# Kernel tuning notes

Hardware: AMD Instinct MI355X
Metric: run time of the kernel (lower is better)

The kernel has to match this reference:

```python
import jax, jax.numpy as jnp
import numpy as np

N_NODES = 100000

def gcn_conv(x, W, b, row, col, n):
    # PyG GCNConv: linear transform, then symmetric-normalized aggregation
    h = x @ W  # [N, out]
    # add self loops
    sl = jnp.arange(n, dtype=row.dtype)
    r = jnp.concatenate([row, sl])
    c = jnp.concatenate([col, sl])
    deg = jax.ops.segment_sum(jnp.ones_like(c, dtype=h.dtype), c, num_segments=n)
    dinv = jnp.where(deg > 0, jax.lax.rsqrt(deg), 0.0)
    norm = dinv[r] * dinv[c]  # [E+N]
    out = jax.ops.segment_sum(h[r] * norm[:, None], c, num_segments=n)
    return out + b


def setup_inputs() -> dict:
    key = jax.random.key(0)
    k1, k2, k3, k4, k5, k6 = jax.random.split(key, 6)
    E = 1600000
    x = jax.random.normal(k1, (N_NODES, 256), dtype=jnp.float32)
    edge_index = jax.random.randint(k2, (2, E), 0, N_NODES, dtype=jnp.int64)
    # Glorot-style init for GCN weights
    W1 = jax.random.normal(k3, (256, 128), dtype=jnp.float32) / np.sqrt(256.0)
    b1 = jnp.zeros((128,), dtype=jnp.float32)
    W2 = jax.random.normal(k4, (128, 64), dtype=jnp.float32) / np.sqrt(128.0)
    b2 = jnp.zeros((64,), dtype=jnp.float32)
    return {"x": x, "edge_index": edge_index, "W1": W1, "b1": b1, "W2": W2, "b2": b2}


def reference(x, edge_index, W1, b1, W2, b2):
    row, col = edge_index[0], edge_index[1]
    h = gcn_conv(x, W1, b1, row, col, N_NODES)
    h = jax.nn.relu(h)
    z = gcn_conv(h, W2, b2, row, col, N_NODES)
    return z
```

## Files before the change

kernel.cpp:

```cpp
#include <hip/hip_runtime.h>

#define NN 100000
#define BW 256
#define NB ((NN + BW - 1) / BW)
#define CH 4096

typedef __attribute__((ext_vector_type(8))) short short8;
typedef __attribute__((ext_vector_type(4))) float f32x4;

__device__ __forceinline__ float bf2f(unsigned short u) {
    union { unsigned int i; float f; } v;
    v.i = ((unsigned int)u) << 16;
    return v.f;
}
__device__ __forceinline__ unsigned short f2bf(float f) {
    unsigned int u = __float_as_uint(f);
    unsigned int r = u + 0x7fffu + ((u >> 16) & 1u);
    return (unsigned short)(r >> 16);
}
__device__ __forceinline__ float ldf(const void* p, int i, int bf) {
    return bf ? bf2f(((const unsigned short*)p)[i]) : ((const float*)p)[i];
}
__device__ __forceinline__ int lde(const void* p, int i, int i64f) {
    return i64f ? (int)((const long long*)p)[i] : ((const int*)p)[i];
}
__device__ __forceinline__ short8 ld8bf(const void* p, size_t i, int bf) {
    if (bf) return *(const short8*)((const unsigned short*)p + i);
    const float* f = (const float*)p + i;
    f32x4 a = *(const f32x4*)f;
    f32x4 b = *(const f32x4*)(f + 4);
    short8 o;
    o[0] = (short)f2bf(a[0]); o[1] = (short)f2bf(a[1]);
    o[2] = (short)f2bf(a[2]); o[3] = (short)f2bf(a[3]);
    o[4] = (short)f2bf(b[0]); o[5] = (short)f2bf(b[1]);
    o[6] = (short)f2bf(b[2]); o[7] = (short)f2bf(b[3]);
    return o;
}

__global__ void detect_kernel(const unsigned int* __restrict__ xw,
                              const unsigned int* __restrict__ eiw,
                              int* __restrict__ flags) {
    __shared__ int s0, s1;
    int tid = threadIdx.x;
    if (tid == 0) { s0 = 0; s1 = 0; }
    __syncthreads();
    if (tid < 128) {
        unsigned int w = xw[tid];
        int e = (int)((w >> 7) & 0xFFu);
        if (e < 100 || e > 130) atomicAdd(&s0, 1);
    } else if (tid < 192) {
        if (eiw[2 * (tid - 128) + 1] == 0u) atomicAdd(&s1, 1);
    }
    __syncthreads();
    if (tid == 0) {
        flags[0] = (s0 < 16) ? 1 : 0;
        flags[1] = (s1 >= 48) ? 1 : 0;
    }
}

__global__ __launch_bounds__(512) void sort_tr_kernel(const void* __restrict__ ei, int E,
                                                      int* __restrict__ bcnt,
                                                      int* __restrict__ poff,
                                                      int* __restrict__ ebin,
                                                      const int* __restrict__ flags,
                                                      const void* __restrict__ w1,
                                                      const void* __restrict__ w2,
                                                      unsigned short* __restrict__ w1t,
                                                      unsigned short* __restrict__ w2t,
                                                      int PB) {
    __shared__ int lc[NB + 1];
    __shared__ int ls[512];
    __shared__ int sbuf[CH];
    int bid = blockIdx.x, tid = threadIdx.x;
    if (bid < PB) {
        int i64f = flags[1];
        int base = bid * CH;
        int cntE = min(CH, E - base);
        int re[CH / 512], ce[CH / 512];
        for (int i = tid; i < NB; i += 512) lc[i] = 0;
        __syncthreads();
#pragma unroll
        for (int q = 0; q < CH / 512; ++q) {
            int e = base + q * 512 + tid;
            if (e < E) {
                int r = lde(ei, e, i64f);
                int c = lde(ei, E + e, i64f);
                r = min(max(r, 0), NN - 1);
                c = min(max(c, 0), NN - 1);
                re[q] = r; ce[q] = c;
                atomicAdd(&lc[c >> 8], 1);
            } else {
                re[q] = -1; ce[q] = 0;
            }
        }
        __syncthreads();
        int v = (tid < NB) ? lc[tid] : 0;
        ls[tid] = v;
        __syncthreads();
        for (int o = 1; o < 512; o <<= 1) {
            int t = (tid >= o) ? ls[tid - o] : 0;
            __syncthreads();
            ls[tid] += t;
            __syncthreads();
        }
        int excl = ls[tid] - v;
        if (tid < NB) {
            poff[bid * (NB + 1) + tid] = excl;
            if (v) atomicAdd(&bcnt[tid], v);
        }
        if (tid == 0) poff[bid * (NB + 1) + NB] = cntE;
        __syncthreads();
        if (tid < NB) lc[tid] = excl;
        __syncthreads();
#pragma unroll
        for (int q = 0; q < CH / 512; ++q) {
            if (re[q] >= 0) {
                int pos = atomicAdd(&lc[ce[q] >> 8], 1);
                sbuf[pos] = (re[q] << 8) | (ce[q] & 255);
            }
        }
        __syncthreads();
        for (int i = tid; i < cntE; i += 512)
            ebin[base + i] = sbuf[i];
    } else {
        int bf = flags[0];
        int i = (bid - PB) * 512 + tid;
        if (i < 128 * 256) {
            int n = i >> 8, k = i & 255;
            w1t[n * 256 + k] = f2bf(ldf(w1, k * 128 + n, bf));
        } else if (i < 128 * 256 + 64 * 128) {
            int j = i - 128 * 256;
            int n = j >> 7, k = j & 127;
            w2t[n * 128 + k] = f2bf(ldf(w2, k * 64 + n, bf));
        }
    }
}

__global__ void bscan_kernel(const int* __restrict__ bcnt, int* __restrict__ bstart,
                             int* __restrict__ off, int E) {
    __shared__ int s[512];
    int tid = threadIdx.x;
    int v = (tid < NB) ? bcnt[tid] : 0;
    s[tid] = v;
    __syncthreads();
    for (int o = 1; o < 512; o <<= 1) {
        int t = (tid >= o) ? s[tid - o] : 0;
        __syncthreads();
        s[tid] += t;
        __syncthreads();
    }
    int excl = s[tid] - v;
    if (tid < NB) bstart[tid] = excl;
    if (tid == NB - 1) bstart[NB] = excl + v;
    if (tid == 0) off[NN] = E;
}

__global__ __launch_bounds__(512) void sg1_kernel(const int* __restrict__ ebin,
                                                  const int* __restrict__ poff,
                                                  const int* __restrict__ bstart,
                                                  int* __restrict__ off,
                                                  float* __restrict__ dinv,
                                                  int* __restrict__ epair,
                                                  const int* __restrict__ flags,
                                                  const void* __restrict__ x,
                                                  const unsigned short* __restrict__ wt,
                                                  unsigned short* __restrict__ h,
                                                  int GB, int PB) {
    __shared__ unsigned short wl[128 * 136];
    __shared__ int cnt[BW], pfx[BW];
    int bid = blockIdx.x, tid = threadIdx.x;
    bool isC = ((bid % 3) == 0) && (bid / 3 < NB);
    if (isC) {
        int b = bid / 3;
        int c0 = b << 8;
        int s = bstart[b];
        for (int i = tid; i < BW; i += 512) cnt[i] = 0;
        __syncthreads();
        for (int p = tid; p < PB; p += 512) {
            const int* pr = poff + p * (NB + 1);
            int s0 = p * CH + pr[b], s1 = p * CH + pr[b + 1];
            for (int i = s0; i < s1; ++i)
                atomicAdd(&cnt[ebin[i] & 255], 1);
        }
        __syncthreads();
        int v = (tid < BW) ? cnt[tid] : 0;
        if (tid < BW) pfx[tid] = v;
        __syncthreads();
        for (int o = 1; o < BW; o <<= 1) {
            int t = (tid < BW && tid >= o) ? pfx[tid - o] : 0;
            __syncthreads();
            if (tid < BW) pfx[tid] += t;
            __syncthreads();
        }
        if (tid < BW) {
            int basec = s + pfx[tid] - v;
            int node = c0 + tid;
            if (node < NN) {
                off[node] = basec;
                dinv[node] = rsqrtf((float)(v + 1));
            }
            cnt[tid] = basec;
        }
        __syncthreads();
        for (int p = tid; p < PB; p += 512) {
            const int* pr = poff + p * (NB + 1);
            int s0 = p * CH + pr[b], s1 = p * CH + pr[b + 1];
            for (int i = s0; i < s1; ++i) {
                int w = ebin[i];
                int pos = atomicAdd(&cnt[w & 255], 1);
                epair[pos] = w >> 8;
            }
        }
        return;
    }
    int gb = bid - min(bid / 3 + 1, NB);
    int bf = flags[0];
    int lane = tid & 63, wv = tid >> 6;
    int ln = lane & 15, kq = lane >> 4;
    int rowBase = gb * 128 + wv * 16;
    int anode = min(rowBase + ln, NN - 1);
    size_t abase = (size_t)anode * 256;
    f32x4 acc[8];
#pragma unroll
    for (int t = 0; t < 8; ++t) acc[t] = (f32x4)0.f;

    for (int half = 0; half < 2; ++half) {
        __syncthreads();
        for (int i = tid; i < 128 * 16; i += 512) {
            int n = i >> 4, b = i & 15;
            short8 v = *(const short8*)(wt + n * 256 + half * 128 + b * 8);
            *(short8*)(&wl[n * 136 + b * 8]) = v;
        }
        __syncthreads();
#pragma unroll
        for (int ks = 0; ks < 4; ++ks) {
            int klocal = ks * 32 + kq * 8;
            short8 a = ld8bf(x, abase + half * 128 + klocal, bf);
#pragma unroll
            for (int t = 0; t < 8; ++t) {
                int n = t * 16 + ln;
                short8 b = *(const short8*)(&wl[n * 136 + klocal]);
                acc[t] = __builtin_amdgcn_mfma_f32_16x16x32_bf16(a, b, acc[t], 0, 0, 0);
            }
        }
    }
#pragma unroll
    for (int r = 0; r < 4; ++r) {
        int node = rowBase + kq * 4 + r;
        if (node < NN) {
            unsigned short* orow = h + (size_t)node * 128;
#pragma unroll
            for (int t = 0; t < 8; ++t)
                orow[t * 16 + ln] = f2bf(acc[t][r]);
        }
    }
}

__global__ __launch_bounds__(256) void ag1_kernel(const unsigned short* __restrict__ h,
                                                  const float* __restrict__ dinv,
                                                  const int* __restrict__ off,
                                                  const int* __restrict__ epair,
                                                  const void* __restrict__ b1,
                                                  const unsigned short* __restrict__ w2t,
                                                  unsigned short* __restrict__ h2,
                                                  const int* __restrict__ flags) {
    __shared__ unsigned short sA[16 * 136];
    int tid = threadIdx.x;
    int lane = tid & 63, wv = tid >> 6;
    int g = lane >> 4, l = lane & 15;
    int cb0 = blockIdx.x * 16;
    int c = cb0 + wv * 4 + g;
    int bf = flags[0];
    float acc[8];
#pragma unroll
    for (int f = 0; f < 8; ++f) acc[f] = 0.f;
    if (c < NN) {
        float dc = dinv[c];
        int jb = off[c], je = off[c + 1];
        {
            short8 v = *(const short8*)(h + (size_t)c * 128 + l * 8);
            float w = dc * dc;
#pragma unroll
            for (int f = 0; f < 8; ++f) acc[f] = bf2f((unsigned short)v[f]) * w;
        }
        int j = jb;
        for (; j + 3 < je; j += 4) {
            int s0 = epair[j], s1 = epair[j + 1], s2 = epair[j + 2], s3 = epair[j + 3];
            float w0 = dinv[s0] * dc, w1 = dinv[s1] * dc;
            float w2 = dinv[s2] * dc, w3 = dinv[s3] * dc;
            short8 v0 = *(const short8*)(h + (size_t)s0 * 128 + l * 8);
            short8 v1 = *(const short8*)(h + (size_t)s1 * 128 + l * 8);
            short8 v2 = *(const short8*)(h + (size_t)s2 * 128 + l * 8);
            short8 v3 = *(const short8*)(h + (size_t)s3 * 128 + l * 8);
#pragma unroll
            for (int f = 0; f < 8; ++f) {
                acc[f] = fmaf(bf2f((unsigned short)v0[f]), w0, acc[f]);
                acc[f] = fmaf(bf2f((unsigned short)v1[f]), w1, acc[f]);
                acc[f] = fmaf(bf2f((unsigned short)v2[f]), w2, acc[f]);
                acc[f] = fmaf(bf2f((unsigned short)v3[f]), w3, acc[f]);
            }
        }
        for (; j < je; ++j) {
            int s0 = epair[j];
            float w = dinv[s0] * dc;
            short8 v = *(const short8*)(h + (size_t)s0 * 128 + l * 8);
#pragma unroll
            for (int f = 0; f < 8; ++f) acc[f] = fmaf(bf2f((unsigned short)v[f]), w, acc[f]);
        }
    }
    {
        short8 o;
#pragma unroll
        for (int f = 0; f < 8; ++f)
            o[f] = (short)f2bf(fmaxf(acc[f] + ldf(b1, l * 8 + f, bf), 0.f));
        *(short8*)(&sA[(wv * 4 + g) * 136 + l * 8]) = o;
    }
    __syncthreads();
    int ln = lane & 15, kq = lane >> 4;
    f32x4 a2 = (f32x4)0.f;
#pragma unroll
    for (int ks = 0; ks < 4; ++ks) {
        int k0 = ks * 32 + kq * 8;
        short8 a = *(const short8*)(&sA[ln * 136 + k0]);
        short8 b = *(const short8*)(w2t + (wv * 16 + ln) * 128 + k0);
        a2 = __builtin_amdgcn_mfma_f32_16x16x32_bf16(a, b, a2, 0, 0, 0);
    }
#pragma unroll
    for (int r = 0; r < 4; ++r) {
        int node = cb0 + kq * 4 + r;
        if (node < NN)
            h2[(size_t)node * 64 + wv * 16 + ln] = f2bf(a2[r]);
    }
}

__global__ __launch_bounds__(256) void agg_out_kernel(const unsigned short* __restrict__ h,
                                                      const float* __restrict__ dinv,
                                                      const int* __restrict__ off,
                                                      const int* __restrict__ epair,
                                                      const void* __restrict__ b2,
                                                      void* __restrict__ outp,
                                                      const int* __restrict__ flags) {
    int tid = threadIdx.x;
    int lane = tid & 63, wv = tid >> 6;
    int g = lane >> 3, l = lane & 7;
    int c = blockIdx.x * 32 + wv * 8 + g;
    if (c >= NN) return;
    int bf = flags[0];
    float dc = dinv[c];
    int jb = off[c], je = off[c + 1];
    float acc[8];
    {
        short8 v = *(const short8*)(h + (size_t)c * 64 + l * 8);
        float w = dc * dc;
#pragma unroll
        for (int f = 0; f < 8; ++f) acc[f] = bf2f((unsigned short)v[f]) * w;
    }
    int j = jb;
    for (; j + 3 < je; j += 4) {
        int s0 = epair[j], s1 = epair[j + 1], s2 = epair[j + 2], s3 = epair[j + 3];
        float w0 = dinv[s0] * dc, w1 = dinv[s1] * dc;
        float w2 = dinv[s2] * dc, w3 = dinv[s3] * dc;
        short8 v0 = *(const short8*)(h + (size_t)s0 * 64 + l * 8);
        short8 v1 = *(const short8*)(h + (size_t)s1 * 64 + l * 8);
        short8 v2 = *(const short8*)(h + (size_t)s2 * 64 + l * 8);
        short8 v3 = *(const short8*)(h + (size_t)s3 * 64 + l * 8);
#pragma unroll
        for (int f = 0; f < 8; ++f) {
            acc[f] = fmaf(bf2f((unsigned short)v0[f]), w0, acc[f]);
            acc[f] = fmaf(bf2f((unsigned short)v1[f]), w1, acc[f]);
            acc[f] = fmaf(bf2f((unsigned short)v2[f]), w2, acc[f]);
            acc[f] = fmaf(bf2f((unsigned short)v3[f]), w3, acc[f]);
        }
    }
    for (; j < je; ++j) {
        int s0 = epair[j];
        float w = dinv[s0] * dc;
        short8 v = *(const short8*)(h + (size_t)s0 * 64 + l * 8);
#pragma unroll
        for (int f = 0; f < 8; ++f) acc[f] = fmaf(bf2f((unsigned short)v[f]), w, acc[f]);
    }
    if (bf) {
        short8 o;
#pragma unroll
        for (int f = 0; f < 8; ++f)
            o[f] = (short)f2bf(acc[f] + ldf(b2, l * 8 + f, 1));
        *(short8*)((unsigned short*)outp + (size_t)c * 64 + l * 8) = o;
    } else {
        float* op = (float*)outp + (size_t)c * 64 + l * 8;
#pragma unroll
        for (int f = 0; f < 8; ++f)
            op[f] = acc[f] + ldf(b2, l * 8 + f, 0);
    }
}

extern "C" void kernel_launch(void* const* d_in, const int* in_sizes, int n_in,
                              void* d_out, int out_size, void* d_ws, size_t ws_size,
                              hipStream_t stream) {
    const void* x  = d_in[0];
    const void* ei = d_in[1];
    const void* W1 = d_in[2];
    const void* b1 = d_in[3];
    const void* W2 = d_in[4];
    const void* b2 = d_in[5];

    const int N = NN;
    const int E = in_sizes[1] / 2;
    const int PB = (E + CH - 1) / CH;
    const int GB = (N + 127) / 128;
    const int TB = (128 * 256 + 64 * 128 + 511) / 512;

    char* ws = (char*)d_ws;
    size_t o = 0;
    auto alloc = [&](size_t bytes) { size_t r = o; o += (bytes + 255) & ~(size_t)255; return r; };
    int*   flags  = (int*)(ws + alloc(256));
    int*   bcnt   = (int*)(ws + alloc((size_t)(NB + 1) * 4));
    int*   bstart = (int*)(ws + alloc((size_t)(NB + 1) * 4));
    int*   off    = (int*)(ws + alloc((size_t)(N + 1) * 4));
    float* dinv   = (float*)(ws + alloc((size_t)N * 4));
    int*   epair  = (int*)(ws + alloc((size_t)E * 4));
    int*   poff   = (int*)(ws + alloc((size_t)PB * (NB + 1) * 4));
    unsigned short* w1t  = (unsigned short*)(ws + alloc(128 * 256 * 2));
    unsigned short* w2t  = (unsigned short*)(ws + alloc(64 * 128 * 2));
    unsigned short* h1   = (unsigned short*)(ws + alloc((size_t)N * 128 * 2));
    unsigned short* buf2 = (unsigned short*)(ws + alloc((size_t)N * 128 * 2));
    unsigned short* h2   = buf2;
    int* ebin = (int*)buf2;

    detect_kernel<<<1, 256, 0, stream>>>((const unsigned int*)x, (const unsigned int*)ei, flags);
    hipMemsetAsync(bcnt, 0, (size_t)(NB + 1) * 4, stream);
    sort_tr_kernel<<<PB + TB, 512, 0, stream>>>(ei, E, bcnt, poff, ebin, flags, W1, W2, w1t, w2t, PB);
    bscan_kernel<<<1, 512, 0, stream>>>(bcnt, bstart, off, E);
    sg1_kernel<<<GB + NB, 512, 0, stream>>>(ebin, poff, bstart, off, dinv, epair, flags, x, w1t, h1, GB, PB);
    ag1_kernel<<<(N + 15) / 16, 256, 0, stream>>>(h1, dinv, off, epair, b1, w2t, h2, flags);
    agg_out_kernel<<<(N + 31) / 32, 256, 0, stream>>>(h2, dinv, off, epair, b2, d_out, flags);
}
```

Before: 335.5 us.

## Fold detect and bucket-scan kernels into neighbors and prefetch GEMM A operands

Removes two tiny single-block kernel launches. Every sort block now recomputes the dtype-detection flags itself, and every count block in sg1 recomputes the bucket prefix scan from bcnt. This drops launch and serialization gaps between stages. In exchange it adds redundant per-block work: 192 global loads in each of roughly 400 sort blocks, and a 512-wide scan in each of roughly 390 count blocks. The GEMM path also loads both halves of the x row into registers ahead of time, so global loads overlap the weight staging to LDS, at the cost of extra register pressure.

Result: faster. 328.4 us (-2.1%).

```diff
diff --git a/kernel.cpp b/kernel.cpp
--- a/kernel.cpp
+++ b/kernel.cpp
@@ -37,32 +37,12 @@
     return o;
 }
 
-__global__ void detect_kernel(const unsigned int* __restrict__ xw,
-                              const unsigned int* __restrict__ eiw,
-                              int* __restrict__ flags) {
-    __shared__ int s0, s1;
-    int tid = threadIdx.x;
-    if (tid == 0) { s0 = 0; s1 = 0; }
-    __syncthreads();
-    if (tid < 128) {
-        unsigned int w = xw[tid];
-        int e = (int)((w >> 7) & 0xFFu);
-        if (e < 100 || e > 130) atomicAdd(&s0, 1);
-    } else if (tid < 192) {
-        if (eiw[2 * (tid - 128) + 1] == 0u) atomicAdd(&s1, 1);
-    }
-    __syncthreads();
-    if (tid == 0) {
-        flags[0] = (s0 < 16) ? 1 : 0;
-        flags[1] = (s1 >= 48) ? 1 : 0;
-    }
-}
-
 __global__ __launch_bounds__(512) void sort_tr_kernel(const void* __restrict__ ei, int E,
                                                       int* __restrict__ bcnt,
                                                       int* __restrict__ poff,
                                                       int* __restrict__ ebin,
-                                                      const int* __restrict__ flags,
+                                                      int* __restrict__ flags,
+                                                      const void* __restrict__ x,
                                                       const void* __restrict__ w1,
                                                       const void* __restrict__ w2,
                                                       unsigned short* __restrict__ w1t,
@@ -71,9 +51,23 @@
     __shared__ int lc[NB + 1];
     __shared__ int ls[512];
     __shared__ int sbuf[CH];
+    __shared__ int sf[2];
     int bid = blockIdx.x, tid = threadIdx.x;
+    if (tid == 0) { sf[0] = 0; sf[1] = 0; }
+    __syncthreads();
+    if (tid < 128) {
+        unsigned int w = ((const unsigned int*)x)[tid];
+        int e = (int)((w >> 7) & 0xFFu);
+        if (e < 100 || e > 130) atomicAdd(&sf[0], 1);
+    } else if (tid < 192) {
+        if (((const unsigned int*)ei)[2 * (tid - 128) + 1] == 0u) atomicAdd(&sf[1], 1);
+    }
+    __syncthreads();
+    int bf = (sf[0] < 16) ? 1 : 0;
+    int i64f = (sf[1] >= 48) ? 1 : 0;
+    if (bid == 0 && tid == 0) { flags[0] = bf; flags[1] = i64f; }
+
     if (bid < PB) {
-        int i64f = flags[1];
         int base = bid * CH;
         int cntE = min(CH, E - base);
         int re[CH / 512], ce[CH / 512];
@@ -123,7 +117,6 @@
         for (int i = tid; i < cntE; i += 512)
             ebin[base + i] = sbuf[i];
     } else {
-        int bf = flags[0];
         int i = (bid - PB) * 512 + tid;
         if (i < 128 * 256) {
             int n = i >> 8, k = i & 255;
@@ -136,28 +129,9 @@
     }
 }
 
-__global__ void bscan_kernel(const int* __restrict__ bcnt, int* __restrict__ bstart,
-                             int* __restrict__ off, int E) {
-    __shared__ int s[512];
-    int tid = threadIdx.x;
-    int v = (tid < NB) ? bcnt[tid] : 0;
-    s[tid] = v;
-    __syncthreads();
-    for (int o = 1; o < 512; o <<= 1) {
-        int t = (tid >= o) ? s[tid - o] : 0;
-        __syncthreads();
-        s[tid] += t;
-        __syncthreads();
-    }
-    int excl = s[tid] - v;
-    if (tid < NB) bstart[tid] = excl;
-    if (tid == NB - 1) bstart[NB] = excl + v;
-    if (tid == 0) off[NN] = E;
-}
-
 __global__ __launch_bounds__(512) void sg1_kernel(const int* __restrict__ ebin,
                                                   const int* __restrict__ poff,
-                                                  const int* __restrict__ bstart,
+                                                  const int* __restrict__ bcnt,
                                                   int* __restrict__ off,
                                                   float* __restrict__ dinv,
                                                   int* __restrict__ epair,
@@ -168,12 +142,23 @@
                                                   int GB, int PB) {
     __shared__ unsigned short wl[128 * 136];
     __shared__ int cnt[BW], pfx[BW];
+    __shared__ int ls2[512];
     int bid = blockIdx.x, tid = threadIdx.x;
     bool isC = ((bid % 3) == 0) && (bid / 3 < NB);
     if (isC) {
         int b = bid / 3;
         int c0 = b << 8;
-        int s = bstart[b];
+        int bv = (tid < NB) ? bcnt[tid] : 0;
+        ls2[tid] = bv;
+        __syncthreads();
+        for (int o = 1; o < 512; o <<= 1) {
+            int t = (tid >= o) ? ls2[tid - o] : 0;
+            __syncthreads();
+            ls2[tid] += t;
+            __syncthreads();
+        }
+        int s = (b > 0) ? ls2[b - 1] : 0;
+        if (b == NB - 1 && tid == 0) off[NN] = ls2[NB - 1];
         for (int i = tid; i < BW; i += 512) cnt[i] = 0;
         __syncthreads();
         for (int p = tid; p < PB; p += 512) {
@@ -220,28 +205,50 @@
     int rowBase = gb * 128 + wv * 16;
     int anode = min(rowBase + ln, NN - 1);
     size_t abase = (size_t)anode * 256;
+    short8 a0[4];
+#pragma unroll
+    for (int q = 0; q < 4; ++q)
+        a0[q] = ld8bf(x, abase + q * 32 + kq * 8, bf);
     f32x4 acc[8];
 #pragma unroll
     for (int t = 0; t < 8; ++t) acc[t] = (f32x4)0.f;
 
-    for (int half = 0; half < 2; ++half) {
-        __syncthreads();
-        for (int i = tid; i < 128 * 16; i += 512) {
-            int n = i >> 4, b = i & 15;
-            short8 v = *(const short8*)(wt + n * 256 + half * 128 + b * 8);
-            *(short8*)(&wl[n * 136 + b * 8]) = v;
-        }
-        __syncthreads();
-#pragma unroll
-        for (int ks = 0; ks < 4; ++ks) {
-            int klocal = ks * 32 + kq * 8;
-            short8 a = ld8bf(x, abase + half * 128 + klocal, bf);
-#pragma unroll
-            for (int t = 0; t < 8; ++t) {
-                int n = t * 16 + ln;
-                short8 b = *(const short8*)(&wl[n * 136 + klocal]);
-                acc[t] = __builtin_amdgcn_mfma_f32_16x16x32_bf16(a, b, acc[t], 0, 0, 0);
-            }
+    __syncthreads();
+    for (int i = tid; i < 128 * 16; i += 512) {
+        int n = i >> 4, b = i & 15;
+        short8 v = *(const short8*)(wt + n * 256 + b * 8);
+        *(short8*)(&wl[n * 136 + b * 8]) = v;
+    }
+    __syncthreads();
+    short8 a1[4];
+#pragma unroll
+    for (int q = 0; q < 4; ++q)
+        a1[q] = ld8bf(x, abase + 128 + q * 32 + kq * 8, bf);
+#pragma unroll
+    for (int ks = 0; ks < 4; ++ks) {
+        int klocal = ks * 32 + kq * 8;
+#pragma unroll
+        for (int t = 0; t < 8; ++t) {
+            int n = t * 16 + ln;
+            short8 b = *(const short8*)(&wl[n * 136 + klocal]);
+            acc[t] = __builtin_amdgcn_mfma_f32_16x16x32_bf16(a0[ks], b, acc[t], 0, 0, 0);
+        }
+    }
+    __syncthreads();
+    for (int i = tid; i < 128 * 16; i += 512) {
+        int n = i >> 4, b = i & 15;
+        short8 v = *(const short8*)(wt + n * 256 + 128 + b * 8);
+        *(short8*)(&wl[n * 136 + b * 8]) = v;
+    }
+    __syncthreads();
+#pragma unroll
+    for (int ks = 0; ks < 4; ++ks) {
+        int klocal = ks * 32 + kq * 8;
+#pragma unroll
+        for (int t = 0; t < 8; ++t) {
+            int n = t * 16 + ln;
+            short8 b = *(const short8*)(&wl[n * 136 + klocal]);
+            acc[t] = __builtin_amdgcn_mfma_f32_16x16x32_bf16(a1[ks], b, acc[t], 0, 0, 0);
         }
     }
 #pragma unroll
@@ -414,7 +421,6 @@
     auto alloc = [&](size_t bytes) { size_t r = o; o += (bytes + 255) & ~(size_t)255; return r; };
     int*   flags  = (int*)(ws + alloc(256));
     int*   bcnt   = (int*)(ws + alloc((size_t)(NB + 1) * 4));
-    int*   bstart = (int*)(ws + alloc((size_t)(NB + 1) * 4));
     int*   off    = (int*)(ws + alloc((size_t)(N + 1) * 4));
     float* dinv   = (float*)(ws + alloc((size_t)N * 4));
     int*   epair  = (int*)(ws + alloc((size_t)E * 4));
@@ -426,11 +432,9 @@
     unsigned short* h2   = buf2;
     int* ebin = (int*)buf2;
 
-    detect_kernel<<<1, 256, 0, stream>>>((const unsigned int*)x, (const unsigned int*)ei, flags);
     hipMemsetAsync(bcnt, 0, (size_t)(NB + 1) * 4, stream);
-    sort_tr_kernel<<<PB + TB, 512, 0, stream>>>(ei, E, bcnt, poff, ebin, flags, W1, W2, w1t, w2t, PB);
-    bscan_kernel<<<1, 512, 0, stream>>>(bcnt, bstart, off, E);
-    sg1_kernel<<<GB + NB, 512, 0, stream>>>(ebin, poff, bstart, off, dinv, epair, flags, x, w1t, h1, GB, PB);
+    sort_tr_kernel<<<PB + TB, 512, 0, stream>>>(ei, E, bcnt, poff, ebin, flags, x, W1, W2, w1t, w2t, PB);
+    sg1_kernel<<<GB + NB, 512, 0, stream>>>(ebin, poff, bcnt, off, dinv, epair, flags, x, w1t, h1, GB, PB);
     ag1_kernel<<<(N + 15) / 16, 256, 0, stream>>>(h1, dinv, off, epair, b1, w2t, h2, flags);
     agg_out_kernel<<<(N + 31) / 32, 256, 0, stream>>>(h2, dinv, off, epair, b2, d_out, flags);
 }
```
